# Performance work log

Hardware: AMD Instinct MI355X
Metric: run time of the kernel (lower is better)

Reference implementation:

```python
import jax, jax.numpy as jnp
import numpy as np

BS, S, D, H = 4, 1024, 768, 12
NE, M, P = 42, 8, 500
IN_C, OUT_C = 3, 256
EMB, BLK, NL = 768, 64, 97


def setup_inputs() -> dict:
    key = jax.random.key(0)
    ks = jax.random.split(key, 16)
    seq_out = jax.random.normal(ks[0], (BS, S, D), jnp.float32)
    attention = jax.random.uniform(ks[1], (BS, H, S, S), jnp.float32)
    ent_tok = jax.random.randint(ks[2], (BS, NE, M), 0, 1022)
    ent_mask = (jax.random.uniform(ks[3], (BS, NE, M)) < 0.7).astype(jnp.float32)
    ent_mask = ent_mask.at[:, :, 0].set(1.0)  # every entity has >=1 mention
    hts = jax.random.randint(ks[4], (BS, P, 2), 0, NE)
    sc = 0.02
    return {
        'seq_out': seq_out,
        'attention': attention,
        'ent_tok': ent_tok,
        'ent_mask': ent_mask,
        'hts': hts,
        'W_liner': jax.random.normal(ks[5], (D, IN_C)) * sc,
        'b_liner': jnp.zeros((IN_C,), jnp.float32),
        'W_seg': jax.random.normal(ks[6], (IN_C, OUT_C)) * sc,
        'b_seg': jnp.zeros((OUT_C,), jnp.float32),
        'W_head': jax.random.normal(ks[7], (D + OUT_C, EMB)) * sc,
        'b_head': jnp.zeros((EMB,), jnp.float32),
        'W_tail': jax.random.normal(ks[8], (D + OUT_C, EMB)) * sc,
        'b_tail': jnp.zeros((EMB,), jnp.float32),
        'W_bil': jax.random.normal(ks[9], (EMB * BLK, NL)) * sc,
        'b_bil': jnp.zeros((NL,), jnp.float32),
    }


def reference(seq_out, attention, ent_tok, ent_mask, hts,
              W_liner, b_liner, W_seg, b_seg,
              W_head, b_head, W_tail, b_tail, W_bil, b_bil):
    bs, S_, d = seq_out.shape
    heads = attention.shape[1]
    # --- get_hrt: per-entity ragged pooling (offset=1 on token starts) ---
    idx = jnp.clip(ent_tok + 1, 0, S_ - 1)                   # [bs,ne,M]
    valid = ent_mask * (ent_tok + 1 < S_).astype(ent_mask.dtype)
    b_ix = jnp.arange(bs)[:, None, None]
    tok_emb = seq_out[b_ix, idx]                             # [bs,ne,M,d]
    neg = jnp.where(valid[..., None] > 0, tok_emb, jnp.float32(-1e30))
    e_emb = jax.nn.logsumexp(neg, axis=2)                    # [bs,ne,d]
    cnt = valid.sum(2)                                       # [bs,ne]
    e_emb = jnp.where((cnt > 0)[..., None], e_emb, 0.0)
    att_g = attention[b_ix, :, idx]                          # [bs,ne,M,H,S]
    e_att = (att_g * valid[..., None, None]).sum(2) / jnp.maximum(cnt, 1.0)[..., None, None]  # [bs,ne,H,S]
    e_att = jnp.where((cnt > 0)[..., None, None], e_att, 0.0)
    # --- get_channel_map: attention-weighted context contraction ---
    ht_att = jnp.einsum('bihs,bjhs->bijs', e_att, e_att) / heads  # [bs,ne,ne,S]
    ht_att = ht_att / (ht_att.sum(-1, keepdims=True) + 1e-5)
    feat = jnp.einsum('bijs,bsd->bijd', ht_att, seq_out)          # [bs,ne,ne,d]
    # --- liner + segmentation stand-in (pointwise) ---
    attn_map = (feat @ W_liner + b_liner) @ W_seg + b_seg         # [bs,ne,ne,OUT_C]
    # --- gather pair features ---
    bp = jnp.arange(bs)[:, None]
    h_i, t_i = hts[..., 0], hts[..., 1]
    h_t = attn_map[bp, h_i, t_i].reshape(-1, attn_map.shape[-1])  # [bs*P,OUT_C]
    hs = e_emb[bp, h_i].reshape(-1, d)
    ts = e_emb[bp, t_i].reshape(-1, d)
    hs = jnp.tanh(jnp.concatenate([hs, h_t], axis=1) @ W_head + b_head)
    ts = jnp.tanh(jnp.concatenate([ts, h_t], axis=1) @ W_tail + b_tail)
    # --- block bilinear classifier ---
    n = hs.shape[0]
    b1 = hs.reshape(n, EMB // BLK, BLK)
    b2 = ts.reshape(n, EMB // BLK, BLK)
    bl = (b1[:, :, :, None] * b2[:, :, None, :]).reshape(n, EMB * BLK)
    logits = bl @ W_bil + b_bil                                   # [bs*P, NL]
    return logits
```

## Files before the change

kernel.cpp:

```cpp
#include <hip/hip_runtime.h>
#include <hip/hip_bf16.h>
#include <math.h>

#define BSZ 4
#define SEQ 1024
#define DIM 768
#define NH 12
#define NEnt 42
#define MM 8
#define PPairs 500
#define INC 3
#define OUTC 256
#define EMB 768
#define BLKsz 64
#define NG 12
#define NL 97
#define NPAIR (BSZ*PPairs)
#define XROWS 2048
#define NCHUNK 24

typedef __bf16 bf16x8 __attribute__((ext_vector_type(8)));
typedef __bf16 bf16x4 __attribute__((ext_vector_type(4)));
typedef float f32x4 __attribute__((ext_vector_type(4)));

#define OFF_EEMB  4096
#define OFF_EATT  520192
#define OFF_SP    4648960
#define OFF_HT    4698112
#define OFF_XB    6746112
#define OFF_HSB   15134720
#define OFF_TSB   18206720
#define OFF_PART  21278720
#define OFF_WHT   520192
#define OFF_WT    4698112

__device__ __forceinline__ float ldin(const void* p, long long i, int f32) {
  if (f32) return ((const float*)p)[i];
  unsigned int u = (unsigned int)(((const unsigned short*)p)[i]) << 16;
  union { unsigned int u; float f; } c; c.u = u;
  return c.f;
}

__device__ __forceinline__ float tanhf_fast(float x) {
  float ax = fabsf(x);
  float t = __expf(-2.0f*ax);
  float r = (1.0f - t)/(1.0f + t);
  return x < 0.0f ? -r : r;
}

__global__ void k_detect(const void* w_head, int* flag) {
  int tid = threadIdx.x;
  unsigned int word = ((const unsigned int*)w_head)[tid];
  union { unsigned int u; float f; } c;
  c.u = (word & 0xFFFFu) << 16;
  float v = fabsf(c.f);
  unsigned long long m = __ballot(v > 1.0f);
  if (tid == 0) flag[0] = (__popcll(m) >= 8) ? 1 : 0;
}

__global__ void k_wT(const void* wbil, const int* flag, __bf16* wT) {
  __shared__ float t[128][98];
  int kb = blockIdx.x, g = blockIdx.y, tid = threadIdx.x;
  int f32 = *flag;
  long long base = ((long long)g*4096 + kb*128)*97;
  for (int i = tid; i < 128*97; i += 256)
    t[i/97][i%97] = ldin(wbil, base + i, f32);
  __syncthreads();
  for (int j = tid; j < 97*128; j += 256) {
    int l = j >> 7, k = j & 127;
    wT[((long long)g*97 + l)*4096 + kb*128 + k] = (__bf16)t[k][l];
  }
}

__global__ void k_whT(const void* whead, const void* wtail, const int* flag,
                      __bf16* whT) {
  __shared__ float t[64][65];
  int kb = blockIdx.x, nb = blockIdx.y, y = blockIdx.z;
  int tid = threadIdx.x;
  int f32 = *flag;
  const void* W = y ? wtail : whead;
  for (int i = tid; i < 64*64; i += 256) {
    int r = i >> 6, c = i & 63;
    t[r][c] = ldin(W, (long long)(kb*64 + r)*EMB + nb*64 + c, f32);
  }
  __syncthreads();
  for (int j = tid; j < 64*64; j += 256) {
    int r = j >> 6, k = j & 63;
    whT[((long long)y*EMB + nb*64 + r)*1024 + kb*64 + k] = (__bf16)t[k][r];
  }
}

__global__ void k_eemb(const void* seq, const int* etok, const void* emask,
                       const int* flag, float* e_emb) {
  int be = blockIdx.x;
  int b = be / NEnt;
  int tid = threadIdx.x;
  int f32 = *flag;
  __shared__ int sidx[MM];
  __shared__ float sval[MM];
  if (tid < MM) {
    int t = etok[be*MM + tid];
    int ip = t + 1;
    float v = ldin(emask, be*MM + tid, f32);
    sval[tid] = (ip < SEQ) ? v : 0.0f;
    int ic = ip < 0 ? 0 : (ip > SEQ-1 ? SEQ-1 : ip);
    sidx[tid] = ic;
  }
  __syncthreads();
  float cnt = 0.0f;
#pragma unroll
  for (int m = 0; m < MM; m++) cnt += sval[m];
  for (int d = tid; d < DIM; d += 256) {
    float x[MM];
#pragma unroll
    for (int m = 0; m < MM; m++)
      x[m] = ldin(seq, ((long long)(b*SEQ) + sidx[m])*DIM + d, f32);
    float mx = -1e30f;
#pragma unroll
    for (int m = 0; m < MM; m++) if (sval[m] > 0.0f && x[m] > mx) mx = x[m];
    float s = 0.0f;
#pragma unroll
    for (int m = 0; m < MM; m++) if (sval[m] > 0.0f) s += expf(x[m] - mx);
    float e = (cnt > 0.0f) ? (mx + logf(s)) : 0.0f;
    e_emb[(long long)be*DIM + d] = e;
  }
}

__global__ void k_eatt(const void* att, const int* etok, const void* emask,
                       const int* flag, __bf16* e_att) {
  int beh = blockIdx.x;
  int h = beh % NH;
  int be = beh / NH;
  int b = be / NEnt;
  int tid = threadIdx.x;
  int f32 = *flag;
  __shared__ int sidx[MM];
  __shared__ float sval[MM];
  if (tid < MM) {
    int t = etok[be*MM + tid];
    int ip = t + 1;
    float v = ldin(emask, be*MM + tid, f32);
    sval[tid] = (ip < SEQ) ? v : 0.0f;
    int ic = ip < 0 ? 0 : (ip > SEQ-1 ? SEQ-1 : ip);
    sidx[tid] = ic;
  }
  __syncthreads();
  float cnt = 0.0f;
#pragma unroll
  for (int m = 0; m < MM; m++) cnt += sval[m];
  float rs = (cnt > 0.0f) ? 1.0f/fmaxf(cnt, 1.0f) : 0.0f;
  long long abase = ((long long)(b*NH + h))*SEQ*SEQ;
  for (int s = tid; s < SEQ; s += 256) {
    float acc = 0.0f;
#pragma unroll
    for (int m = 0; m < MM; m++)
      if (sval[m] > 0.0f)
        acc += sval[m]*ldin(att, abase + (long long)sidx[m]*SEQ + s, f32);
    e_att[((long long)be*SEQ + s)*NH + h] = (__bf16)(acc*rs);
  }
}

__global__ void k_sp(const void* seq, const void* wliner, const int* flag,
                     float* sp) {
  int bs = blockIdx.x;
  int tid = threadIdx.x;
  int f32 = *flag;
  float a0 = 0, a1 = 0, a2 = 0;
  for (int d = tid; d < DIM; d += 256) {
    float x = ldin(seq, (long long)bs*DIM + d, f32);
    a0 += x*ldin(wliner, (long long)d*3 + 0, f32);
    a1 += x*ldin(wliner, (long long)d*3 + 1, f32);
    a2 += x*ldin(wliner, (long long)d*3 + 2, f32);
  }
  __shared__ float r0[256], r1[256], r2[256];
  r0[tid] = a0; r1[tid] = a1; r2[tid] = a2;
  __syncthreads();
  for (int o = 128; o > 0; o >>= 1) {
    if (tid < o) { r0[tid] += r0[tid+o]; r1[tid] += r1[tid+o]; r2[tid] += r2[tid+o]; }
    __syncthreads();
  }
  if (tid == 0) {
    sp[bs*3 + 0] = r0[0]; sp[bs*3 + 1] = r1[0]; sp[bs*3 + 2] = r2[0];
  }
}

__global__ void k_pair(const __bf16* e_att, const float* sp, const int* hts,
                       const void* bliner, const void* wseg, const void* bseg,
                       const int* flag, float* h_t) {
  int p = blockIdx.x;
  int b = p / PPairs;
  int tid = threadIdx.x;
  int f32 = *flag;
  int hi = hts[p*2 + 0];
  int ti = hts[p*2 + 1];
  const __bf16* ei = e_att + (long long)(b*NEnt + hi)*SEQ*NH;
  const __bf16* ej = e_att + (long long)(b*NEnt + ti)*SEQ*NH;
  float dn = 0, a0 = 0, a1 = 0, a2 = 0;
  for (int s = tid; s < SEQ; s += 256) {
    const __bf16* pi = ei + s*NH;
    const __bf16* pj = ej + s*NH;
    float q = 0.0f;
#pragma unroll
    for (int v = 0; v < 3; v++) {
      bf16x4 xi = *(const bf16x4*)(pi + v*4);
      bf16x4 xj = *(const bf16x4*)(pj + v*4);
#pragma unroll
      for (int h = 0; h < 4; h++) q += (float)xi[h]*(float)xj[h];
    }
    q *= (1.0f/NH);
    dn += q;
    a0 += q*sp[(b*SEQ + s)*3 + 0];
    a1 += q*sp[(b*SEQ + s)*3 + 1];
    a2 += q*sp[(b*SEQ + s)*3 + 2];
  }
  __shared__ float red[4][256];
  red[0][tid] = dn; red[1][tid] = a0; red[2][tid] = a1; red[3][tid] = a2;
  __syncthreads();
  for (int o = 128; o > 0; o >>= 1) {
    if (tid < o) {
      red[0][tid] += red[0][tid+o];
      red[1][tid] += red[1][tid+o];
      red[2][tid] += red[2][tid+o];
      red[3][tid] += red[3][tid+o];
    }
    __syncthreads();
  }
  float scale = 1.0f/(red[0][0] + 1e-5f);
  float v0 = red[1][0]*scale + ldin(bliner, 0, f32);
  float v1 = red[2][0]*scale + ldin(bliner, 1, f32);
  float v2 = red[3][0]*scale + ldin(bliner, 2, f32);
  float o = ldin(bseg, tid, f32)
          + v0*ldin(wseg, 0*OUTC + tid, f32)
          + v1*ldin(wseg, 1*OUTC + tid, f32)
          + v2*ldin(wseg, 2*OUTC + tid, f32);
  h_t[(long long)p*OUTC + tid] = o;
}

__global__ void k_buildx(const float* e_emb, const float* h_t, const int* hts,
                         __bf16* Xb) {
  int p = blockIdx.x;
  int y = blockIdx.y;
  int tid = threadIdx.x;
  __bf16* dst = Xb + ((long long)y*XROWS + p)*1024;
  if (p >= NPAIR) {
    for (int k = tid; k < 1024; k += 256) dst[k] = (__bf16)0.0f;
    return;
  }
  int b = p / PPairs;
  int ent = hts[p*2 + y];
  const float* er = e_emb + (long long)(b*NEnt + ent)*DIM;
  for (int k = tid; k < 1024; k += 256) {
    float v = (k < DIM) ? er[k] : h_t[(long long)p*OUTC + (k - DIM)];
    dst[k] = (__bf16)v;
  }
}

__global__ __launch_bounds__(128, 2)
void k_htmm(const __bf16* Xb, const __bf16* whT,
            const void* bhead, const void* btail, const int* flag,
            __bf16* hsb, __bf16* tsb) {
  __shared__ __bf16 Xa[2][128][72];
  __shared__ __bf16 Bb[2][64][72];
  int tid = threadIdx.x;
  int w = tid >> 6, lane = tid & 63, quad = lane >> 4, col = lane & 15;
  int m0 = blockIdx.x*128;
  int n0 = blockIdx.y*64;
  int y  = blockIdx.z;
  int f32 = *flag;
  const __bf16* Xg = Xb + (long long)y*XROWS*1024;
  const __bf16* Wg = whT + ((long long)y*EMB + n0)*1024;

  auto stage = [&](int kk, int p) {
#pragma unroll
    for (int it = 0; it < 8; it++) {
      int r = (tid >> 3) + 16*it;
      int c0 = (tid & 7)*8;
      bf16x8 v = *(const bf16x8*)(Xg + (long long)(m0 + r)*1024 + kk + c0);
      *(bf16x8*)&Xa[p][r][c0] = v;
    }
#pragma unroll
    for (int it = 0; it < 4; it++) {
      int r = tid >> 1;
      int c0 = (tid & 1)*32 + it*8;
      bf16x8 v = *(const bf16x8*)(Wg + (long long)r*1024 + kk + c0);
      *(bf16x8*)&Bb[p][r][c0] = v;
    }
  };

  f32x4 acc[4][4];
#pragma unroll
  for (int mf = 0; mf < 4; mf++)
#pragma unroll
    for (int nt = 0; nt < 4; nt++) acc[mf][nt] = (f32x4){0,0,0,0};

  stage(0, 0);
  __syncthreads();
  for (int c = 0; c < 16; c++) {
    int p = c & 1;
    if (c + 1 < 16) stage((c+1)*64, p ^ 1);
#pragma unroll
    for (int s = 0; s < 2; s++) {
      bf16x8 av[4], bv[4];
#pragma unroll
      for (int mf = 0; mf < 4; mf++)
        av[mf] = *(bf16x8*)&Xa[p][w*64 + mf*16 + col][s*32 + quad*8];
#pragma unroll
      for (int nt = 0; nt < 4; nt++)
        bv[nt] = *(bf16x8*)&Bb[p][nt*16 + col][s*32 + quad*8];
#pragma unroll
      for (int mf = 0; mf < 4; mf++)
#pragma unroll
        for (int nt = 0; nt < 4; nt++)
          acc[mf][nt] = __builtin_amdgcn_mfma_f32_16x16x32_bf16(av[mf], bv[nt],
                                                                acc[mf][nt], 0, 0, 0);
    }
    __syncthreads();
  }

  const void* Bv = y ? btail : bhead;
  __bf16* out = y ? tsb : hsb;
#pragma unroll
  for (int nt = 0; nt < 4; nt++) {
    int n = n0 + nt*16 + col;
    float bias = ldin(Bv, n, f32);
#pragma unroll
    for (int mf = 0; mf < 4; mf++)
#pragma unroll
      for (int reg = 0; reg < 4; reg++) {
        int m = m0 + w*64 + mf*16 + quad*4 + reg;
        if (m < NPAIR)
          out[(long long)m*EMB + n] = (__bf16)tanhf_fast(acc[mf][nt][reg] + bias);
      }
  }
}

__global__ __launch_bounds__(128, 2)
void k_bilmfma(const __bf16* hsb, const __bf16* tsb,
               const __bf16* wT, _Float16* part24) {
  __shared__ __bf16 hslT[32][136];
  int tid = threadIdx.x;
  int w = tid >> 6, lane = tid & 63, quad = lane >> 4, col = lane & 15;
  int m0 = blockIdx.x*128;
  int c  = blockIdx.y;
  int g  = c >> 1, kh = c & 1;

  {
    int row = m0 + tid; if (row > NPAIR-1) row = NPAIR-1;
    const __bf16* hp = hsb + (long long)row*EMB + g*BLKsz + kh*32;
#pragma unroll
    for (int c0 = 0; c0 < 4; c0++) {
      bf16x8 hv = *(const bf16x8*)(hp + c0*8);
#pragma unroll
      for (int j = 0; j < 8; j++) hslT[c0*8 + j][tid] = hv[j];
    }
  }
  bf16x8 tsv[4][2];
#pragma unroll
  for (int mf = 0; mf < 4; mf++) {
    int row = m0 + w*64 + mf*16 + col; if (row > NPAIR-1) row = NPAIR-1;
    const __bf16* tp = tsb + (long long)row*EMB + g*BLKsz + quad*8;
    tsv[mf][0] = *(const bf16x8*)(tp);
    tsv[mf][1] = *(const bf16x8*)(tp + 32);
  }
  __syncthreads();

  const __bf16* wg = wT + (long long)g*NL*4096 + kh*2048 + quad*8;
  int boff[7];
#pragma unroll
  for (int nt = 0; nt < 7; nt++) {
    int l = nt*16 + col; if (l > 96) l = 96;
    boff[nt] = l*4096;
  }
  f32x4 acc[4][7];
#pragma unroll
  for (int mf = 0; mf < 4; mf++)
#pragma unroll
    for (int nt = 0; nt < 7; nt++) acc[mf][nt] = (f32x4){0,0,0,0};

  bf16x8 bv[2][7];
#pragma unroll
  for (int nt = 0; nt < 7; nt++) bv[0][nt] = *(const bf16x8*)(wg + boff[nt]);
#pragma unroll
  for (int nt = 0; nt < 7; nt++) bv[1][nt] = *(const bf16x8*)(wg + boff[nt] + 32);

  for (int a = 0; a < 32; a++) {
    float hv[4];
#pragma unroll
    for (int mf = 0; mf < 4; mf++)
      hv[mf] = (float)hslT[a][w*64 + mf*16 + col];
#pragma unroll
    for (int half = 0; half < 2; half++) {
      bf16x8 af[4];
#pragma unroll
      for (int mf = 0; mf < 4; mf++)
#pragma unroll
        for (int j = 0; j < 8; j++)
          af[mf][j] = (__bf16)(hv[mf] * (float)tsv[mf][half][j]);
#pragma unroll
      for (int mf = 0; mf < 4; mf++)
#pragma unroll
        for (int nt = 0; nt < 7; nt++)
          acc[mf][nt] = __builtin_amdgcn_mfma_f32_16x16x32_bf16(af[mf], bv[half][nt],
                                                                acc[mf][nt], 0, 0, 0);
      int knext = (a+1)*64 + half*32;
      if (knext >= 2048) knext = a*64 + half*32;
#pragma unroll
      for (int nt = 0; nt < 7; nt++)
        bv[half][nt] = *(const bf16x8*)(wg + boff[nt] + knext);
    }
  }

  _Float16* ps = part24 + (long long)c*NPAIR*NL;
#pragma unroll
  for (int mf = 0; mf < 4; mf++)
#pragma unroll
    for (int nt = 0; nt < 7; nt++)
#pragma unroll
      for (int reg = 0; reg < 4; reg++) {
        int n = m0 + w*64 + mf*16 + quad*4 + reg;
        int l = nt*16 + col;
        if (n < NPAIR && l < NL)
          ps[(long long)n*NL + l] = (_Float16)acc[mf][nt][reg];
      }
}

__global__ void k_final(const _Float16* part24, const void* b_bil, const int* flag,
                        void* out) {
  int i = blockIdx.x*256 + threadIdx.x;
  if (i >= NPAIR*NL) return;
  int l = i % NL;
  int f32 = *flag;
  float v = ldin(b_bil, l, f32);
#pragma unroll
  for (int c = 0; c < NCHUNK; c++) v += (float)part24[(long long)c*NPAIR*NL + i];
  if (f32) ((float*)out)[i] = v;
  else ((__hip_bfloat16*)out)[i] = __float2bfloat16(v);
}

extern "C" void kernel_launch(void* const* d_in, const int* in_sizes, int n_in,
                              void* d_out, int out_size, void* d_ws, size_t ws_size,
                              hipStream_t stream) {
  const void* seq    = d_in[0];
  const void* att    = d_in[1];
  const int*  etok   = (const int*)d_in[2];
  const void* emask  = d_in[3];
  const int*  hts    = (const int*)d_in[4];
  const void* wliner = d_in[5];
  const void* bliner = d_in[6];
  const void* wseg   = d_in[7];
  const void* bseg   = d_in[8];
  const void* whead  = d_in[9];
  const void* bhead  = d_in[10];
  const void* wtail  = d_in[11];
  const void* btail  = d_in[12];
  const void* wbil   = d_in[13];
  const void* bbil   = d_in[14];

  char* ws = (char*)d_ws;
  int*      flag   = (int*)ws;
  float*    e_emb  = (float*)(ws + OFF_EEMB);
  __bf16*   e_att  = (__bf16*)(ws + OFF_EATT);
  float*    sp     = (float*)(ws + OFF_SP);
  float*    h_t    = (float*)(ws + OFF_HT);
  __bf16*   Xb     = (__bf16*)(ws + OFF_XB);
  __bf16*   hsb    = (__bf16*)(ws + OFF_HSB);
  __bf16*   tsb    = (__bf16*)(ws + OFF_TSB);
  _Float16* part24 = (_Float16*)(ws + OFF_PART);
  __bf16*   whT    = (__bf16*)(ws + OFF_WHT);
  __bf16*   wT     = (__bf16*)(ws + OFF_WT);

  k_detect<<<1, 64, 0, stream>>>(whead, flag);
  k_eemb<<<BSZ*NEnt, 256, 0, stream>>>(seq, etok, emask, flag, e_emb);
  k_eatt<<<BSZ*NEnt*NH, 256, 0, stream>>>(att, etok, emask, flag, e_att);
  k_sp<<<BSZ*SEQ, 256, 0, stream>>>(seq, wliner, flag, sp);
  k_pair<<<NPAIR, 256, 0, stream>>>(e_att, sp, hts, bliner, wseg, bseg, flag, h_t);
  k_buildx<<<dim3(XROWS, 2), 256, 0, stream>>>(e_emb, h_t, hts, Xb);
  k_whT<<<dim3(16, 12, 2), 256, 0, stream>>>(whead, wtail, flag, whT);
  k_htmm<<<dim3(16, 12, 2), 128, 0, stream>>>(Xb, whT, bhead, btail, flag, hsb, tsb);
  k_wT<<<dim3(32, 12), 256, 0, stream>>>(wbil, flag, wT);
  k_bilmfma<<<dim3(16, NCHUNK), 128, 0, stream>>>(hsb, tsb, wT, part24);
  k_final<<<(NPAIR*NL + 255)/256, 256, 0, stream>>>(part24, bbil, flag, d_out);
}
```

Measured before the change: 456.9 us.

## Fuse prep kernels into one launch, reshape e_att layout, retile MFMA kernels

Merges the entity pooling, attention pooling, seq projection and both weight transposes into a single multi-role k_stage1 launch, and folds pair-feature building into k_pair2. e_att is stored head-major so pair dot products use vectorized contiguous loads, with wave-shuffle reductions replacing shared-memory trees. k_htmm moves to 256 threads with smaller per-wave tiles, and k_bilmfma uses 64-row blocks to double grid parallelism. This cuts launch count and serialization and raises occupancy, at the cost of a heterogeneous fused kernel whose roles may be load-imbalanced.

```diff
diff --git a/kernel.cpp b/kernel.cpp
--- a/kernel.cpp
+++ b/kernel.cpp
@@ -13,7 +13,6 @@
 #define OUTC 256
 #define EMB 768
 #define BLKsz 64
-#define NG 12
 #define NL 97
 #define NPAIR (BSZ*PPairs)
 #define XROWS 2048
@@ -26,19 +25,41 @@
 #define OFF_EEMB  4096
 #define OFF_EATT  520192
 #define OFF_SP    4648960
-#define OFF_HT    4698112
-#define OFF_XB    6746112
-#define OFF_HSB   15134720
-#define OFF_TSB   18206720
-#define OFF_PART  21278720
-#define OFF_WHT   520192
-#define OFF_WT    4698112
+#define OFF_XB    4698112
+#define OFF_WHT   13086720
+#define OFF_WT    16232448
+#define OFF_HSB   25767936
+#define OFF_TSB   28839936
+#define OFF_PART  31911936
+
+#define B_EEMB0 0
+#define B_EATT0 168
+#define B_SP0   2184
+#define B_WHT0  3208
+#define B_WT0   3592
+#define B_ZERO0 4360
+#define B_TOTAL 4362
 
 __device__ __forceinline__ float ldin(const void* p, long long i, int f32) {
   if (f32) return ((const float*)p)[i];
   unsigned int u = (unsigned int)(((const unsigned short*)p)[i]) << 16;
   union { unsigned int u; float f; } c; c.u = u;
   return c.f;
+}
+
+__device__ __forceinline__ f32x4 ldin4(const void* p, long long i, int f32) {
+  f32x4 r;
+  if (f32) {
+    r = *(const f32x4*)((const float*)p + i);
+  } else {
+    unsigned long long v = *(const unsigned long long*)((const unsigned short*)p + i);
+    union { unsigned int u; float f; } c;
+    c.u = (unsigned int)(v & 0xFFFFu) << 16;         r[0] = c.f;
+    c.u = (unsigned int)((v >> 16) & 0xFFFFu) << 16; r[1] = c.f;
+    c.u = (unsigned int)((v >> 32) & 0xFFFFu) << 16; r[2] = c.f;
+    c.u = (unsigned int)((v >> 48) & 0xFFFFu) << 16; r[3] = c.f;
+  }
+  return r;
 }
 
 __device__ __forceinline__ float tanhf_fast(float x) {
@@ -58,204 +79,200 @@
   if (tid == 0) flag[0] = (__popcll(m) >= 8) ? 1 : 0;
 }
 
-__global__ void k_wT(const void* wbil, const int* flag, __bf16* wT) {
-  __shared__ float t[128][98];
-  int kb = blockIdx.x, g = blockIdx.y, tid = threadIdx.x;
-  int f32 = *flag;
-  long long base = ((long long)g*4096 + kb*128)*97;
-  for (int i = tid; i < 128*97; i += 256)
-    t[i/97][i%97] = ldin(wbil, base + i, f32);
-  __syncthreads();
-  for (int j = tid; j < 97*128; j += 256) {
-    int l = j >> 7, k = j & 127;
-    wT[((long long)g*97 + l)*4096 + kb*128 + k] = (__bf16)t[k][l];
-  }
-}
-
-__global__ void k_whT(const void* whead, const void* wtail, const int* flag,
-                      __bf16* whT) {
-  __shared__ float t[64][65];
-  int kb = blockIdx.x, nb = blockIdx.y, y = blockIdx.z;
+__global__ __launch_bounds__(256)
+void k_stage1(const void* seq, const void* att, const int* etok,
+              const void* emask, const void* wliner,
+              const void* whead, const void* wtail, const void* wbil,
+              const int* flag,
+              float* e_emb, __bf16* e_att, float* sp,
+              __bf16* whT, __bf16* wT, __bf16* Xb) {
+  __shared__ float smem[64*98];
+  int blk = blockIdx.x;
   int tid = threadIdx.x;
   int f32 = *flag;
-  const void* W = y ? wtail : whead;
-  for (int i = tid; i < 64*64; i += 256) {
-    int r = i >> 6, c = i & 63;
-    t[r][c] = ldin(W, (long long)(kb*64 + r)*EMB + nb*64 + c, f32);
-  }
-  __syncthreads();
-  for (int j = tid; j < 64*64; j += 256) {
-    int r = j >> 6, k = j & 63;
-    whT[((long long)y*EMB + nb*64 + r)*1024 + kb*64 + k] = (__bf16)t[k][r];
-  }
-}
-
-__global__ void k_eemb(const void* seq, const int* etok, const void* emask,
-                       const int* flag, float* e_emb) {
-  int be = blockIdx.x;
-  int b = be / NEnt;
-  int tid = threadIdx.x;
-  int f32 = *flag;
-  __shared__ int sidx[MM];
-  __shared__ float sval[MM];
-  if (tid < MM) {
-    int t = etok[be*MM + tid];
-    int ip = t + 1;
-    float v = ldin(emask, be*MM + tid, f32);
-    sval[tid] = (ip < SEQ) ? v : 0.0f;
-    int ic = ip < 0 ? 0 : (ip > SEQ-1 ? SEQ-1 : ip);
-    sidx[tid] = ic;
-  }
-  __syncthreads();
-  float cnt = 0.0f;
-#pragma unroll
-  for (int m = 0; m < MM; m++) cnt += sval[m];
-  for (int d = tid; d < DIM; d += 256) {
-    float x[MM];
+
+  if (blk < B_EATT0) {
+    int be = blk, b = be / NEnt;
+    int* sidx = (int*)smem;
+    float* sval = smem + 16;
+    if (tid < MM) {
+      int t = etok[be*MM + tid];
+      int ip = t + 1;
+      float v = ldin(emask, be*MM + tid, f32);
+      sval[tid] = (ip < SEQ) ? v : 0.0f;
+      sidx[tid] = ip < 0 ? 0 : (ip > SEQ-1 ? SEQ-1 : ip);
+    }
+    __syncthreads();
+    float cnt = 0.0f;
+#pragma unroll
+    for (int m = 0; m < MM; m++) cnt += sval[m];
+    for (int d = tid; d < DIM; d += 256) {
+      float x[MM];
+#pragma unroll
+      for (int m = 0; m < MM; m++)
+        x[m] = ldin(seq, ((long long)(b*SEQ) + sidx[m])*DIM + d, f32);
+      float mx = -1e30f;
+#pragma unroll
+      for (int m = 0; m < MM; m++) if (sval[m] > 0.0f && x[m] > mx) mx = x[m];
+      float s = 0.0f;
+#pragma unroll
+      for (int m = 0; m < MM; m++) if (sval[m] > 0.0f) s += expf(x[m] - mx);
+      e_emb[(long long)be*DIM + d] = (cnt > 0.0f) ? (mx + logf(s)) : 0.0f;
+    }
+  } else if (blk < B_SP0) {
+    int t1 = blk - B_EATT0;
+    int h = t1 % NH, be = t1 / NH, b = be / NEnt;
+    int* sidx = (int*)smem;
+    float* sval = smem + 16;
+    if (tid < MM) {
+      int t = etok[be*MM + tid];
+      int ip = t + 1;
+      float v = ldin(emask, be*MM + tid, f32);
+      sval[tid] = (ip < SEQ) ? v : 0.0f;
+      sidx[tid] = ip < 0 ? 0 : (ip > SEQ-1 ? SEQ-1 : ip);
+    }
+    __syncthreads();
+    float cnt = 0.0f;
+#pragma unroll
+    for (int m = 0; m < MM; m++) cnt += sval[m];
+    float rs = (cnt > 0.0f) ? 1.0f/fmaxf(cnt, 1.0f) : 0.0f;
+    long long abase = ((long long)(b*NH + h))*SEQ*SEQ;
+    int s0 = tid*4;
+    f32x4 acc = (f32x4){0,0,0,0};
 #pragma unroll
     for (int m = 0; m < MM; m++)
-      x[m] = ldin(seq, ((long long)(b*SEQ) + sidx[m])*DIM + d, f32);
-    float mx = -1e30f;
-#pragma unroll
-    for (int m = 0; m < MM; m++) if (sval[m] > 0.0f && x[m] > mx) mx = x[m];
-    float s = 0.0f;
-#pragma unroll
-    for (int m = 0; m < MM; m++) if (sval[m] > 0.0f) s += expf(x[m] - mx);
-    float e = (cnt > 0.0f) ? (mx + logf(s)) : 0.0f;
-    e_emb[(long long)be*DIM + d] = e;
-  }
-}
-
-__global__ void k_eatt(const void* att, const int* etok, const void* emask,
-                       const int* flag, __bf16* e_att) {
-  int beh = blockIdx.x;
-  int h = beh % NH;
-  int be = beh / NH;
-  int b = be / NEnt;
-  int tid = threadIdx.x;
-  int f32 = *flag;
-  __shared__ int sidx[MM];
-  __shared__ float sval[MM];
-  if (tid < MM) {
-    int t = etok[be*MM + tid];
-    int ip = t + 1;
-    float v = ldin(emask, be*MM + tid, f32);
-    sval[tid] = (ip < SEQ) ? v : 0.0f;
-    int ic = ip < 0 ? 0 : (ip > SEQ-1 ? SEQ-1 : ip);
-    sidx[tid] = ic;
-  }
-  __syncthreads();
-  float cnt = 0.0f;
-#pragma unroll
-  for (int m = 0; m < MM; m++) cnt += sval[m];
-  float rs = (cnt > 0.0f) ? 1.0f/fmaxf(cnt, 1.0f) : 0.0f;
-  long long abase = ((long long)(b*NH + h))*SEQ*SEQ;
-  for (int s = tid; s < SEQ; s += 256) {
-    float acc = 0.0f;
-#pragma unroll
-    for (int m = 0; m < MM; m++)
-      if (sval[m] > 0.0f)
-        acc += sval[m]*ldin(att, abase + (long long)sidx[m]*SEQ + s, f32);
-    e_att[((long long)be*SEQ + s)*NH + h] = (__bf16)(acc*rs);
-  }
-}
-
-__global__ void k_sp(const void* seq, const void* wliner, const int* flag,
-                     float* sp) {
-  int bs = blockIdx.x;
-  int tid = threadIdx.x;
-  int f32 = *flag;
-  float a0 = 0, a1 = 0, a2 = 0;
-  for (int d = tid; d < DIM; d += 256) {
-    float x = ldin(seq, (long long)bs*DIM + d, f32);
-    a0 += x*ldin(wliner, (long long)d*3 + 0, f32);
-    a1 += x*ldin(wliner, (long long)d*3 + 1, f32);
-    a2 += x*ldin(wliner, (long long)d*3 + 2, f32);
-  }
-  __shared__ float r0[256], r1[256], r2[256];
-  r0[tid] = a0; r1[tid] = a1; r2[tid] = a2;
-  __syncthreads();
-  for (int o = 128; o > 0; o >>= 1) {
-    if (tid < o) { r0[tid] += r0[tid+o]; r1[tid] += r1[tid+o]; r2[tid] += r2[tid+o]; }
+      if (sval[m] > 0.0f) {
+        f32x4 v = ldin4(att, abase + (long long)sidx[m]*SEQ + s0, f32);
+        acc += sval[m]*v;
+      }
+    bf16x4 ov;
+#pragma unroll
+    for (int k = 0; k < 4; k++) ov[k] = (__bf16)(acc[k]*rs);
+    *(bf16x4*)(e_att + ((long long)(be*NH + h))*SEQ + s0) = ov;
+  } else if (blk < B_WHT0) {
+    int t2 = blk - B_SP0;
+    int b = t2 >> 8;
+    int wv = tid >> 6, l = tid & 63;
+    int s = ((t2 & 255) << 2) + wv;
+    long long rb = ((long long)(b*SEQ) + s)*DIM;
+    float a0 = 0, a1 = 0, a2 = 0;
+#pragma unroll
+    for (int i = 0; i < DIM/64; i++) {
+      int d = l + i*64;
+      float x = ldin(seq, rb + d, f32);
+      a0 += x*ldin(wliner, (long long)d*3 + 0, f32);
+      a1 += x*ldin(wliner, (long long)d*3 + 1, f32);
+      a2 += x*ldin(wliner, (long long)d*3 + 2, f32);
+    }
+#pragma unroll
+    for (int o = 32; o; o >>= 1) {
+      a0 += __shfl_down(a0, o);
+      a1 += __shfl_down(a1, o);
+      a2 += __shfl_down(a2, o);
+    }
+    if (l == 0) {
+      sp[0*(BSZ*SEQ) + b*SEQ + s] = a0;
+      sp[1*(BSZ*SEQ) + b*SEQ + s] = a1;
+      sp[2*(BSZ*SEQ) + b*SEQ + s] = a2;
+    }
+  } else if (blk < B_WT0) {
+    int t3 = blk - B_WHT0;
+    int kb = t3 & 15, rest = t3 >> 4;
+    int nb = rest % 12, y = rest / 12;
+    const void* W = y ? wtail : whead;
+    for (int i = tid; i < 64*64; i += 256) {
+      int r = i >> 6, c = i & 63;
+      smem[r*65 + c] = ldin(W, (long long)(kb*64 + r)*EMB + nb*64 + c, f32);
+    }
     __syncthreads();
-  }
-  if (tid == 0) {
-    sp[bs*3 + 0] = r0[0]; sp[bs*3 + 1] = r1[0]; sp[bs*3 + 2] = r2[0];
-  }
-}
-
-__global__ void k_pair(const __bf16* e_att, const float* sp, const int* hts,
-                       const void* bliner, const void* wseg, const void* bseg,
-                       const int* flag, float* h_t) {
+    for (int j = tid; j < 64*64; j += 256) {
+      int r = j >> 6, k = j & 63;
+      whT[((long long)y*EMB + nb*64 + r)*1024 + kb*64 + k] = (__bf16)smem[k*65 + r];
+    }
+  } else if (blk < B_ZERO0) {
+    int t4 = blk - B_WT0;
+    int kb = t4 & 63, g = t4 >> 6;
+    long long base = ((long long)g*4096 + kb*64)*97;
+    for (int i = tid; i < 64*97; i += 256)
+      smem[(i/97)*98 + (i%97)] = ldin(wbil, base + i, f32);
+    __syncthreads();
+    for (int j = tid; j < 97*64; j += 256) {
+      int l = j >> 6, k = j & 63;
+      wT[((long long)g*97 + l)*4096 + kb*64 + k] = (__bf16)smem[k*98 + l];
+    }
+  } else {
+    int y = blk - B_ZERO0;
+    uint4 z = {0,0,0,0};
+    uint4* dst = (uint4*)(Xb + ((long long)(y*XROWS + NPAIR))*1024);
+    for (int i = tid; i < 48*1024*2/16; i += 256) dst[i] = z;
+  }
+}
+
+__global__ __launch_bounds__(256)
+void k_pair2(const __bf16* e_att, const float* sp, const float* e_emb,
+             const int* hts, const void* bliner, const void* wseg,
+             const void* bseg, const int* flag, __bf16* Xb) {
+  __shared__ float cross[4][4];
   int p = blockIdx.x;
   int b = p / PPairs;
   int tid = threadIdx.x;
   int f32 = *flag;
   int hi = hts[p*2 + 0];
   int ti = hts[p*2 + 1];
-  const __bf16* ei = e_att + (long long)(b*NEnt + hi)*SEQ*NH;
-  const __bf16* ej = e_att + (long long)(b*NEnt + ti)*SEQ*NH;
-  float dn = 0, a0 = 0, a1 = 0, a2 = 0;
-  for (int s = tid; s < SEQ; s += 256) {
-    const __bf16* pi = ei + s*NH;
-    const __bf16* pj = ej + s*NH;
-    float q = 0.0f;
-#pragma unroll
-    for (int v = 0; v < 3; v++) {
-      bf16x4 xi = *(const bf16x4*)(pi + v*4);
-      bf16x4 xj = *(const bf16x4*)(pj + v*4);
-#pragma unroll
-      for (int h = 0; h < 4; h++) q += (float)xi[h]*(float)xj[h];
-    }
-    q *= (1.0f/NH);
-    dn += q;
-    a0 += q*sp[(b*SEQ + s)*3 + 0];
-    a1 += q*sp[(b*SEQ + s)*3 + 1];
-    a2 += q*sp[(b*SEQ + s)*3 + 2];
-  }
-  __shared__ float red[4][256];
-  red[0][tid] = dn; red[1][tid] = a0; red[2][tid] = a1; red[3][tid] = a2;
+  const __bf16* ei = e_att + ((long long)(b*NEnt + hi))*NH*SEQ;
+  const __bf16* ej = e_att + ((long long)(b*NEnt + ti))*NH*SEQ;
+  int s0 = tid*4;
+  f32x4 q = (f32x4){0,0,0,0};
+#pragma unroll
+  for (int h = 0; h < NH; h++) {
+    bf16x4 xi = *(const bf16x4*)(ei + h*SEQ + s0);
+    bf16x4 xj = *(const bf16x4*)(ej + h*SEQ + s0);
+#pragma unroll
+    for (int k = 0; k < 4; k++) q[k] += (float)xi[k]*(float)xj[k];
+  }
+  f32x4 w0 = *(const f32x4*)(sp + 0*(BSZ*SEQ) + b*SEQ + s0);
+  f32x4 w1 = *(const f32x4*)(sp + 1*(BSZ*SEQ) + b*SEQ + s0);
+  f32x4 w2 = *(const f32x4*)(sp + 2*(BSZ*SEQ) + b*SEQ + s0);
+  float dn = q[0]+q[1]+q[2]+q[3];
+  float a0 = q[0]*w0[0]+q[1]*w0[1]+q[2]*w0[2]+q[3]*w0[3];
+  float a1 = q[0]*w1[0]+q[1]*w1[1]+q[2]*w1[2]+q[3]*w1[3];
+  float a2 = q[0]*w2[0]+q[1]*w2[1]+q[2]*w2[2]+q[3]*w2[3];
+#pragma unroll
+  for (int o = 32; o; o >>= 1) {
+    dn += __shfl_down(dn, o);
+    a0 += __shfl_down(a0, o);
+    a1 += __shfl_down(a1, o);
+    a2 += __shfl_down(a2, o);
+  }
+  int wv = tid >> 6, l = tid & 63;
+  if (l == 0) { cross[0][wv] = dn; cross[1][wv] = a0; cross[2][wv] = a1; cross[3][wv] = a2; }
   __syncthreads();
-  for (int o = 128; o > 0; o >>= 1) {
-    if (tid < o) {
-      red[0][tid] += red[0][tid+o];
-      red[1][tid] += red[1][tid+o];
-      red[2][tid] += red[2][tid+o];
-      red[3][tid] += red[3][tid+o];
-    }
-    __syncthreads();
-  }
-  float scale = 1.0f/(red[0][0] + 1e-5f);
-  float v0 = red[1][0]*scale + ldin(bliner, 0, f32);
-  float v1 = red[2][0]*scale + ldin(bliner, 1, f32);
-  float v2 = red[3][0]*scale + ldin(bliner, 2, f32);
+  float DN = cross[0][0]+cross[0][1]+cross[0][2]+cross[0][3];
+  float A0 = cross[1][0]+cross[1][1]+cross[1][2]+cross[1][3];
+  float A1 = cross[2][0]+cross[2][1]+cross[2][2]+cross[2][3];
+  float A2 = cross[3][0]+cross[3][1]+cross[3][2]+cross[3][3];
+  const float inv = 1.0f/(float)NH;
+  float scale = inv/(DN*inv + 1e-5f);
+  float v0 = A0*scale + ldin(bliner, 0, f32);
+  float v1 = A1*scale + ldin(bliner, 1, f32);
+  float v2 = A2*scale + ldin(bliner, 2, f32);
   float o = ldin(bseg, tid, f32)
           + v0*ldin(wseg, 0*OUTC + tid, f32)
           + v1*ldin(wseg, 1*OUTC + tid, f32)
           + v2*ldin(wseg, 2*OUTC + tid, f32);
-  h_t[(long long)p*OUTC + tid] = o;
-}
-
-__global__ void k_buildx(const float* e_emb, const float* h_t, const int* hts,
-                         __bf16* Xb) {
-  int p = blockIdx.x;
-  int y = blockIdx.y;
-  int tid = threadIdx.x;
-  __bf16* dst = Xb + ((long long)y*XROWS + p)*1024;
-  if (p >= NPAIR) {
-    for (int k = tid; k < 1024; k += 256) dst[k] = (__bf16)0.0f;
-    return;
-  }
-  int b = p / PPairs;
-  int ent = hts[p*2 + y];
-  const float* er = e_emb + (long long)(b*NEnt + ent)*DIM;
-  for (int k = tid; k < 1024; k += 256) {
-    float v = (k < DIM) ? er[k] : h_t[(long long)p*OUTC + (k - DIM)];
-    dst[k] = (__bf16)v;
-  }
-}
-
-__global__ __launch_bounds__(128, 2)
+  __bf16* X0 = Xb + ((long long)(0*XROWS + p))*1024;
+  __bf16* X1 = Xb + ((long long)(1*XROWS + p))*1024;
+  X0[DIM + tid] = (__bf16)o;
+  X1[DIM + tid] = (__bf16)o;
+  const float* eh = e_emb + (long long)(b*NEnt + hi)*DIM;
+  const float* et = e_emb + (long long)(b*NEnt + ti)*DIM;
+  for (int k = tid; k < DIM; k += 256) {
+    X0[k] = (__bf16)eh[k];
+    X1[k] = (__bf16)et[k];
+  }
+}
+
+__global__ __launch_bounds__(256, 1)
 void k_htmm(const __bf16* Xb, const __bf16* whT,
             const void* bhead, const void* btail, const int* flag,
             __bf16* hsb, __bf16* tsb) {
@@ -272,24 +289,24 @@
 
   auto stage = [&](int kk, int p) {
 #pragma unroll
-    for (int it = 0; it < 8; it++) {
-      int r = (tid >> 3) + 16*it;
+    for (int it = 0; it < 4; it++) {
+      int r = (tid >> 3) + it*32;
       int c0 = (tid & 7)*8;
       bf16x8 v = *(const bf16x8*)(Xg + (long long)(m0 + r)*1024 + kk + c0);
       *(bf16x8*)&Xa[p][r][c0] = v;
     }
 #pragma unroll
-    for (int it = 0; it < 4; it++) {
-      int r = tid >> 1;
-      int c0 = (tid & 1)*32 + it*8;
+    for (int it = 0; it < 2; it++) {
+      int r = (tid >> 3) + it*32;
+      int c0 = (tid & 7)*8;
       bf16x8 v = *(const bf16x8*)(Wg + (long long)r*1024 + kk + c0);
       *(bf16x8*)&Bb[p][r][c0] = v;
     }
   };
 
-  f32x4 acc[4][4];
-#pragma unroll
-  for (int mf = 0; mf < 4; mf++)
+  f32x4 acc[2][4];
+#pragma unroll
+  for (int mf = 0; mf < 2; mf++)
 #pragma unroll
     for (int nt = 0; nt < 4; nt++) acc[mf][nt] = (f32x4){0,0,0,0};
 
@@ -300,15 +317,15 @@
     if (c + 1 < 16) stage((c+1)*64, p ^ 1);
 #pragma unroll
     for (int s = 0; s < 2; s++) {
-      bf16x8 av[4], bv[4];
-#pragma unroll
-      for (int mf = 0; mf < 4; mf++)
-        av[mf] = *(bf16x8*)&Xa[p][w*64 + mf*16 + col][s*32 + quad*8];
+      bf16x8 av[2], bv[4];
+#pragma unroll
+      for (int mf = 0; mf < 2; mf++)
+        av[mf] = *(bf16x8*)&Xa[p][w*32 + mf*16 + col][s*32 + quad*8];
 #pragma unroll
       for (int nt = 0; nt < 4; nt++)
         bv[nt] = *(bf16x8*)&Bb[p][nt*16 + col][s*32 + quad*8];
 #pragma unroll
-      for (int mf = 0; mf < 4; mf++)
+      for (int mf = 0; mf < 2; mf++)
 #pragma unroll
         for (int nt = 0; nt < 4; nt++)
           acc[mf][nt] = __builtin_amdgcn_mfma_f32_16x16x32_bf16(av[mf], bv[nt],
@@ -324,10 +341,10 @@
     int n = n0 + nt*16 + col;
     float bias = ldin(Bv, n, f32);
 #pragma unroll
-    for (int mf = 0; mf < 4; mf++)
+    for (int mf = 0; mf < 2; mf++)
 #pragma unroll
       for (int reg = 0; reg < 4; reg++) {
-        int m = m0 + w*64 + mf*16 + quad*4 + reg;
+        int m = m0 + w*32 + mf*16 + quad*4 + reg;
         if (m < NPAIR)
           out[(long long)m*EMB + n] = (__bf16)tanhf_fast(acc[mf][nt][reg] + bias);
       }
@@ -337,27 +354,29 @@
 __global__ __launch_bounds__(128, 2)
 void k_bilmfma(const __bf16* hsb, const __bf16* tsb,
                const __bf16* wT, _Float16* part24) {
-  __shared__ __bf16 hslT[32][136];
+  __shared__ __bf16 hslT[32][72];
   int tid = threadIdx.x;
   int w = tid >> 6, lane = tid & 63, quad = lane >> 4, col = lane & 15;
-  int m0 = blockIdx.x*128;
+  int m0 = blockIdx.x*64;
   int c  = blockIdx.y;
   int g  = c >> 1, kh = c & 1;
 
   {
-    int row = m0 + tid; if (row > NPAIR-1) row = NPAIR-1;
-    const __bf16* hp = hsb + (long long)row*EMB + g*BLKsz + kh*32;
-#pragma unroll
-    for (int c0 = 0; c0 < 4; c0++) {
+    int srow = tid & 63;
+    int grow = m0 + srow; if (grow > NPAIR-1) grow = NPAIR-1;
+    int ah = (tid >> 6)*16;
+    const __bf16* hp = hsb + (long long)grow*EMB + g*BLKsz + kh*32 + ah;
+#pragma unroll
+    for (int c0 = 0; c0 < 2; c0++) {
       bf16x8 hv = *(const bf16x8*)(hp + c0*8);
 #pragma unroll
-      for (int j = 0; j < 8; j++) hslT[c0*8 + j][tid] = hv[j];
-    }
-  }
-  bf16x8 tsv[4][2];
-#pragma unroll
-  for (int mf = 0; mf < 4; mf++) {
-    int row = m0 + w*64 + mf*16 + col; if (row > NPAIR-1) row = NPAIR-1;
+      for (int j = 0; j < 8; j++) hslT[ah + c0*8 + j][srow] = hv[j];
+    }
+  }
+  bf16x8 tsv[2][2];
+#pragma unroll
+  for (int mf = 0; mf < 2; mf++) {
+    int row = m0 + w*32 + mf*16 + col; if (row > NPAIR-1) row = NPAIR-1;
     const __bf16* tp = tsb + (long long)row*EMB + g*BLKsz + quad*8;
     tsv[mf][0] = *(const bf16x8*)(tp);
     tsv[mf][1] = *(const bf16x8*)(tp + 32);
@@ -371,9 +390,9 @@
     int l = nt*16 + col; if (l > 96) l = 96;
     boff[nt] = l*4096;
   }
-  f32x4 acc[4][7];
-#pragma unroll
-  for (int mf = 0; mf < 4; mf++)
+  f32x4 acc[2][7];
+#pragma unroll
+  for (int mf = 0; mf < 2; mf++)
 #pragma unroll
     for (int nt = 0; nt < 7; nt++) acc[mf][nt] = (f32x4){0,0,0,0};
 
@@ -384,20 +403,20 @@
   for (int nt = 0; nt < 7; nt++) bv[1][nt] = *(const bf16x8*)(wg + boff[nt] + 32);
 
   for (int a = 0; a < 32; a++) {
-    float hv[4];
-#pragma unroll
-    for (int mf = 0; mf < 4; mf++)
-      hv[mf] = (float)hslT[a][w*64 + mf*16 + col];
+    float hv[2];
+#pragma unroll
+    for (int mf = 0; mf < 2; mf++)
+      hv[mf] = (float)hslT[a][w*32 + mf*16 + col];
 #pragma unroll
     for (int half = 0; half < 2; half++) {
-      bf16x8 af[4];
-#pragma unroll
-      for (int mf = 0; mf < 4; mf++)
+      bf16x8 af[2];
+#pragma unroll
+      for (int mf = 0; mf < 2; mf++)
 #pragma unroll
         for (int j = 0; j < 8; j++)
           af[mf][j] = (__bf16)(hv[mf] * (float)tsv[mf][half][j]);
 #pragma unroll
-      for (int mf = 0; mf < 4; mf++)
+      for (int mf = 0; mf < 2; mf++)
 #pragma unroll
         for (int nt = 0; nt < 7; nt++)
           acc[mf][nt] = __builtin_amdgcn_mfma_f32_16x16x32_bf16(af[mf], bv[half][nt],
@@ -412,12 +431,12 @@
 
   _Float16* ps = part24 + (long long)c*NPAIR*NL;
 #pragma unroll
-  for (int mf = 0; mf < 4; mf++)
+  for (int mf = 0; mf < 2; mf++)
 #pragma unroll
     for (int nt = 0; nt < 7; nt++)
 #pragma unroll
       for (int reg = 0; reg < 4; reg++) {
-        int n = m0 + w*64 + mf*16 + quad*4 + reg;
+        int n = m0 + w*32 + mf*16 + quad*4 + reg;
         int l = nt*16 + col;
         if (n < NPAIR && l < NL)
           ps[(long long)n*NL + l] = (_Float16)acc[mf][nt][reg];
@@ -461,23 +480,20 @@
   float*    e_emb  = (float*)(ws + OFF_EEMB);
   __bf16*   e_att  = (__bf16*)(ws + OFF_EATT);
   float*    sp     = (float*)(ws + OFF_SP);
-  float*    h_t    = (float*)(ws + OFF_HT);
   __bf16*   Xb     = (__bf16*)(ws + OFF_XB);
+  __bf16*   whT    = (__bf16*)(ws + OFF_WHT);
+  __bf16*   wT     = (__bf16*)(ws + OFF_WT);
   __bf16*   hsb    = (__bf16*)(ws + OFF_HSB);
   __bf16*   tsb    = (__bf16*)(ws + OFF_TSB);
   _Float16* part24 = (_Float16*)(ws + OFF_PART);
-  __bf16*   whT    = (__bf16*)(ws + OFF_WHT);
-  __bf16*   wT     = (__bf16*)(ws + OFF_WT);
 
   k_detect<<<1, 64, 0, stream>>>(whead, flag);
-  k_eemb<<<BSZ*NEnt, 256, 0, stream>>>(seq, etok, emask, flag, e_emb);
-  k_eatt<<<BSZ*NEnt*NH, 256, 0, stream>>>(att, etok, emask, flag, e_att);
-  k_sp<<<BSZ*SEQ, 256, 0, stream>>>(seq, wliner, flag, sp);
-  k_pair<<<NPAIR, 256, 0, stream>>>(e_att, sp, hts, bliner, wseg, bseg, flag, h_t);
-  k_buildx<<<dim3(XROWS, 2), 256, 0, stream>>>(e_emb, h_t, hts, Xb);
-  k_whT<<<dim3(16, 12, 2), 256, 0, stream>>>(whead, wtail, flag, whT);
-  k_htmm<<<dim3(16, 12, 2), 128, 0, stream>>>(Xb, whT, bhead, btail, flag, hsb, tsb);
-  k_wT<<<dim3(32, 12), 256, 0, stream>>>(wbil, flag, wT);
-  k_bilmfma<<<dim3(16, NCHUNK), 128, 0, stream>>>(hsb, tsb, wT, part24);
+  k_stage1<<<B_TOTAL, 256, 0, stream>>>(seq, att, etok, emask, wliner,
+                                        whead, wtail, wbil, flag,
+                                        e_emb, e_att, sp, whT, wT, Xb);
+  k_pair2<<<NPAIR, 256, 0, stream>>>(e_att, sp, e_emb, hts, bliner, wseg, bseg,
+                                     flag, Xb);
+  k_htmm<<<dim3(16, 12, 2), 256, 0, stream>>>(Xb, whT, bhead, btail, flag, hsb, tsb);
+  k_bilmfma<<<dim3(32, NCHUNK), 128, 0, stream>>>(hsb, tsb, wT, part24);
   k_final<<<(NPAIR*NL + 255)/256, 256, 0, stream>>>(part24, bbil, flag, d_out);
 }
```

Measured after the change: 418.9 us. 1.09x faster.
